# Performance work log

Measured on AMD Instinct MI355X. Metric: run time of the kernel, lower is better.

## Reference

```python
import jax, jax.numpy as jnp
import numpy as np

B, N, C = 4, 100000, 64
S = 256            # img_size
RADIUS_PX = 1.5    # radius in pixels
K = 8              # points_per_pixel
GAMMA = 1.0
R_NDC = RADIUS_PX / S * 2.0  # radius in NDC, as in forward()


def setup_inputs() -> dict:
    key = jax.random.key(0)
    k1, k2 = jax.random.split(key)
    pts = jax.random.normal(k1, (B, N, 3), dtype=jnp.float32)
    features = jax.random.normal(k2, (B, N, C), dtype=jnp.float32)
    return {"pts": pts, "features": features}


def _rasterize_one(pts_b):
    # pts_b: (N,3) sign-flipped NDC points. Emulates pytorch3d rasterize_points:
    # per pixel keep the K nearest-in-z points whose NDC distance to the pixel
    # center is <= R_NDC (points with z < 0 are culled).
    x, y, z = pts_b[:, 0], pts_b[:, 1], pts_b[:, 2]
    # pytorch3d NDC->pixel: ndc = 1 - 2*(p+0.5)/S  =>  p = (1-ndc)*S/2 - 0.5
    px = (1.0 - x) * (S / 2.0) - 0.5
    py = (1.0 - y) * (S / 2.0) - 0.5
    offs = jnp.arange(-1, 3)  # 4-wide window fully covers a 1.5px radius
    cj = jnp.floor(px).astype(jnp.int32)[:, None] + offs  # (N,4) candidate cols
    ci = jnp.floor(py).astype(jnp.int32)[:, None] + offs  # (N,4) candidate rows
    cx = 1.0 - 2.0 * (cj.astype(pts_b.dtype) + 0.5) / S   # pixel-center NDC x
    cy = 1.0 - 2.0 * (ci.astype(pts_b.dtype) + 0.5) / S   # pixel-center NDC y
    d2 = (cy - y[:, None])[:, :, None] ** 2 + (cx - x[:, None])[:, None, :] ** 2  # (N,4,4)
    pid = ci[:, :, None] * S + cj[:, None, :]                                      # (N,4,4)
    inb = (ci[:, :, None] >= 0) & (ci[:, :, None] < S) & (cj[:, None, :] >= 0) & (cj[:, None, :] < S)
    valid = inb & (d2 <= R_NDC * R_NDC) & (z[:, None, None] >= 0.0)
    pid = jnp.where(valid, pid, S * S).reshape(-1)
    zc = jnp.where(valid, z[:, None, None], jnp.inf).reshape(-1)
    d2f = d2.reshape(-1)
    pidx = jnp.broadcast_to(jnp.arange(N, dtype=jnp.int32)[:, None, None], (N, 4, 4)).reshape(-1)
    order = jnp.lexsort((zc, pid))  # sort by pixel id, then depth (front first)
    pid_s, d2_s, pi_s = pid[order], d2f[order], pidx[order]
    seg_start = jnp.searchsorted(pid_s, pid_s, side='left')
    rank = jnp.arange(pid_s.shape[0]) - seg_start  # per-pixel z-rank
    keep = (pid_s < S * S) & (rank < K)
    pid_w = jnp.where(keep, pid_s, S * S)          # OOB index -> dropped by mode='drop'
    rank_w = jnp.where(keep, rank, 0)
    idx_buf = jnp.full((S * S, K), -1, jnp.int32).at[pid_w, rank_w].set(pi_s, mode='drop')
    d_buf = jnp.zeros((S * S, K), pts_b.dtype).at[pid_w, rank_w].set(d2_s, mode='drop')
    return idx_buf.reshape(S, S, K), d_buf.reshape(S, S, K)


def _forward(pts, features):
    # forward() flips x and y signs in-place
    pts = pts * jnp.array([-1.0, -1.0, 1.0], dtype=pts.dtype)
    idx, d2 = jax.vmap(_rasterize_one)(pts)        # (B,S,S,K) each
    dist = d2 / (R_NDC * R_NDC)
    alphas = 1.0 - jnp.clip(dist, 0.001, 1.0) ** (0.5 * GAMMA)  # .pow(0.5).pow(gamma)
    alphas = jnp.where(idx >= 0, alphas, 0.0)      # alpha_composite skips idx < 0
    trans = jnp.cumprod(1.0 - alphas, axis=-1)     # transmittance, front-to-back
    trans = jnp.concatenate([jnp.ones_like(trans[..., :1]), trans[..., :-1]], axis=-1)
    w = alphas * trans                             # (B,S,S,K) compositing weights
    gath = jax.vmap(lambda f, i: f[jnp.clip(i, 0)])(features, idx)  # (B,S,S,K,C)
    return jnp.einsum('bhwk,bhwkc->bchw', w, gath)  # (B,C,S,S)


def reference(pts, features):
    return _forward(pts, features)
```

## Files before the change

kernel.cpp:

```cpp
#include <hip/hip_runtime.h>
#include <stdint.h>

#pragma clang fp contract(off)

#define S 256
#define NPTS 100000
#define BATCH 4
#define CCH 64
#define K 8

static constexpr float R2 = 0.01171875f * 0.01171875f;
static constexpr unsigned long long SENT = 0xFFFFFFFFFFFFFFFFULL;

__global__ void scatter_kernel(const float* __restrict__ pts,
                               unsigned long long* __restrict__ keys) {
    int gid = blockIdx.x * blockDim.x + threadIdx.x;
    if (gid >= BATCH * NPTS) return;
    int b = gid / NPTS;
    int n = gid - b * NPTS;

    const float* p = pts + (size_t)gid * 3;
    float x = -p[0];
    float y = -p[1];
    float z = p[2];
    if (!(z >= 0.0f)) return;

    float px = (1.0f - x) * 128.0f - 0.5f;
    float py = (1.0f - y) * 128.0f - 0.5f;
    int cj0 = (int)floorf(px);
    int ci0 = (int)floorf(py);
    if (ci0 < -2 || ci0 > S || cj0 < -2 || cj0 > S) return;

    unsigned long long zkey =
        ((unsigned long long)__float_as_uint(z) << 32) | (unsigned int)n;
    unsigned long long* kb = keys + (size_t)b * S * S * K;

    for (int a = 0; a < 4; ++a) {
        int ci = ci0 - 1 + a;
        if (ci < 0 || ci >= S) continue;
        float cy = 1.0f - 2.0f * ((float)ci + 0.5f) / 256.0f;
        float dy = cy - y;
        float dy2 = dy * dy;
        for (int d = 0; d < 4; ++d) {
            int cj = cj0 - 1 + d;
            if (cj < 0 || cj >= S) continue;
            float cx = 1.0f - 2.0f * ((float)cj + 0.5f) / 256.0f;
            float dx = cx - x;
            float dx2 = dx * dx;
            float d2 = dy2 + dx2;
            if (d2 <= R2) {
                unsigned long long key = zkey;
                unsigned long long* slot = kb + (size_t)(ci * S + cj) * K;
                for (int s = 0; s < K; ++s) {
                    if (key == SENT) break;
                    unsigned long long old = atomicMin(&slot[s], key);
                    key = old > key ? old : key;
                }
            }
        }
    }
}

__global__ __launch_bounds__(256) void blend_kernel(
        const float* __restrict__ pts,
        const float* __restrict__ feat,
        const unsigned long long* __restrict__ keys,
        float* __restrict__ out) {
    int seg = blockIdx.x;
    int h   = blockIdx.y;
    int b   = blockIdx.z;
    int tid = threadIdx.x;
    int w0  = seg * 64;

    __shared__ float s_alpha[64][K + 1];
    __shared__ float s_wgt[64][K + 1];
    __shared__ int   s_idx[64][K + 1];
    __shared__ int   s_cnt[64];

    const unsigned long long* kb =
        keys + ((size_t)b * S * S + (size_t)h * S + w0) * K;
    const float* pb = pts + (size_t)b * NPTS * 3;

    for (int e = tid; e < 64 * K; e += 256) {
        int p = e >> 3;
        int k = e & 7;
        unsigned long long key = kb[(size_t)p * K + k];
        float alpha = 0.0f;
        int idx = -1;
        if (key != SENT) {
            idx = (int)(unsigned int)(key & 0xFFFFFFFFULL);
            float x = -pb[(size_t)idx * 3 + 0];
            float y = -pb[(size_t)idx * 3 + 1];
            int w = w0 + p;
            float cy = 1.0f - 2.0f * ((float)h + 0.5f) / 256.0f;
            float cx = 1.0f - 2.0f * ((float)w + 0.5f) / 256.0f;
            float dy = cy - y;
            float dx = cx - x;
            float d2 = dy * dy + dx * dx;
            float dist = d2 / R2;
            dist = fminf(fmaxf(dist, 0.001f), 1.0f);
            alpha = 1.0f - sqrtf(dist);
        }
        s_alpha[p][k] = alpha;
        s_idx[p][k] = idx;
    }
    __syncthreads();

    if (tid < 64) {
        float t = 1.0f;
        int cnt = 0;
        for (int k = 0; k < K; ++k) {
            int raw = s_idx[tid][k];
            float a = s_alpha[tid][k];
            s_wgt[tid][k] = a * t;
            t *= (1.0f - a);
            if (raw >= 0) cnt = k + 1;
            s_idx[tid][k] = raw < 0 ? 0 : raw;
        }
        s_cnt[tid] = cnt;
    }
    __syncthreads();

    int wave = tid >> 6;
    int lane = tid & 63;
    int pbase = wave * 16;

    int kmax = 0;
#pragma unroll
    for (int i = 0; i < 16; ++i) {
        int c = s_cnt[pbase + i];
        kmax = c > kmax ? c : kmax;
    }

    float acc[16];
#pragma unroll
    for (int i = 0; i < 16; ++i) acc[i] = 0.0f;

    const float* fbl = feat + (size_t)b * NPTS * CCH + lane;
    for (int k = 0; k < kmax; ++k) {
        float v[16];
#pragma unroll
        for (int i = 0; i < 16; ++i) {
            int idx = s_idx[pbase + i][k];
            v[i] = fbl[(size_t)idx << 6];
        }
#pragma unroll
        for (int i = 0; i < 16; ++i) {
            acc[i] += s_wgt[pbase + i][k] * v[i];
        }
    }

    size_t obase = (((size_t)b * CCH + lane) * S + h) * S + (size_t)(w0 + pbase);
    float4* o4 = (float4*)(out + obase);
#pragma unroll
    for (int q = 0; q < 4; ++q) {
        o4[q] = make_float4(acc[4 * q + 0], acc[4 * q + 1],
                            acc[4 * q + 2], acc[4 * q + 3]);
    }
}

extern "C" void kernel_launch(void* const* d_in, const int* in_sizes, int n_in,
                              void* d_out, int out_size, void* d_ws, size_t ws_size,
                              hipStream_t stream) {
    const float* pts  = (const float*)d_in[0];
    const float* feat = (const float*)d_in[1];
    float* out = (float*)d_out;

    unsigned long long* keys = (unsigned long long*)d_ws;
    size_t key_bytes = (size_t)BATCH * S * S * K * sizeof(unsigned long long);
    hipMemsetAsync(keys, 0xFF, key_bytes, stream);

    int total = BATCH * NPTS;
    scatter_kernel<<<(total + 255) / 256, 256, 0, stream>>>(pts, keys);

    dim3 grid(S / 64, S, BATCH);
    blend_kernel<<<grid, 256, 0, stream>>>(pts, feat, keys, out);
}
```

Measured before the change: 277.7 us.

## Parallelize scatter over 16 window cells and early-exit on full pixel slots

The scatter kernel now launches one thread per point-cell pair (16 per point) instead of looping over the 4x4 window inside one thread, which spreads the serial atomicMin insertion chains across more threads. It also adds a plain read of the last slot and skips the atomic insertion when that slot already holds a smaller key. Each point's coordinates are now loaded by 16 threads, and the pre-check reads a value that other threads may be changing. It is safe because slots only decrease, so any skipped key would have been rejected anyway.

```diff
diff --git a/kernel.cpp b/kernel.cpp
--- a/kernel.cpp
+++ b/kernel.cpp
@@ -12,14 +12,17 @@
 static constexpr float R2 = 0.01171875f * 0.01171875f;
 static constexpr unsigned long long SENT = 0xFFFFFFFFFFFFFFFFULL;
 
-__global__ void scatter_kernel(const float* __restrict__ pts,
-                               unsigned long long* __restrict__ keys) {
+__global__ __launch_bounds__(256) void scatter_kernel(
+        const float* __restrict__ pts,
+        unsigned long long* __restrict__ keys) {
     int gid = blockIdx.x * blockDim.x + threadIdx.x;
-    if (gid >= BATCH * NPTS) return;
-    int b = gid / NPTS;
-    int n = gid - b * NPTS;
+    if (gid >= BATCH * NPTS * 16) return;
+    int cell = gid & 15;
+    int pid  = gid >> 4;
+    int b = pid / NPTS;
+    int n = pid - b * NPTS;
 
-    const float* p = pts + (size_t)gid * 3;
+    const float* p = pts + (size_t)pid * 3;
     float x = -p[0];
     float y = -p[1];
     float z = p[2];
@@ -29,35 +32,29 @@
     float py = (1.0f - y) * 128.0f - 0.5f;
     int cj0 = (int)floorf(px);
     int ci0 = (int)floorf(py);
-    if (ci0 < -2 || ci0 > S || cj0 < -2 || cj0 > S) return;
 
-    unsigned long long zkey =
+    int ci = ci0 - 1 + (cell >> 2);
+    int cj = cj0 - 1 + (cell & 3);
+    if (ci < 0 || ci >= S || cj < 0 || cj >= S) return;
+
+    float cy = 1.0f - 2.0f * ((float)ci + 0.5f) / 256.0f;
+    float cx = 1.0f - 2.0f * ((float)cj + 0.5f) / 256.0f;
+    float dy = cy - y;
+    float dx = cx - x;
+    float d2 = dy * dy + dx * dx;
+    if (!(d2 <= R2)) return;
+
+    unsigned long long key =
         ((unsigned long long)__float_as_uint(z) << 32) | (unsigned int)n;
-    unsigned long long* kb = keys + (size_t)b * S * S * K;
+    unsigned long long* slot =
+        keys + ((size_t)b * S * S + (size_t)(ci * S + cj)) * K;
 
-    for (int a = 0; a < 4; ++a) {
-        int ci = ci0 - 1 + a;
-        if (ci < 0 || ci >= S) continue;
-        float cy = 1.0f - 2.0f * ((float)ci + 0.5f) / 256.0f;
-        float dy = cy - y;
-        float dy2 = dy * dy;
-        for (int d = 0; d < 4; ++d) {
-            int cj = cj0 - 1 + d;
-            if (cj < 0 || cj >= S) continue;
-            float cx = 1.0f - 2.0f * ((float)cj + 0.5f) / 256.0f;
-            float dx = cx - x;
-            float dx2 = dx * dx;
-            float d2 = dy2 + dx2;
-            if (d2 <= R2) {
-                unsigned long long key = zkey;
-                unsigned long long* slot = kb + (size_t)(ci * S + cj) * K;
-                for (int s = 0; s < K; ++s) {
-                    if (key == SENT) break;
-                    unsigned long long old = atomicMin(&slot[s], key);
-                    key = old > key ? old : key;
-                }
-            }
-        }
+    if (slot[K - 1] < key) return;
+
+    for (int s = 0; s < K; ++s) {
+        if (key == SENT) break;
+        unsigned long long old = atomicMin(&slot[s], key);
+        key = old > key ? old : key;
     }
 }
 
@@ -170,7 +167,7 @@
     size_t key_bytes = (size_t)BATCH * S * S * K * sizeof(unsigned long long);
     hipMemsetAsync(keys, 0xFF, key_bytes, stream);
 
-    int total = BATCH * NPTS;
+    int total = BATCH * NPTS * 16;
     scatter_kernel<<<(total + 255) / 256, 256, 0, stream>>>(pts, keys);
 
     dim3 grid(S / 64, S, BATCH);
```

Measured after the change: 274.2 us. No clear change (-1.3%).

## Replace per-pixel atomic top-K scatter with tile binning and shared-memory top-K

Applied to the files above, without the earlier changes.

The fill kernel now bins each visible point into 16x16 pixel tiles, using one atomic counter per tile and a fixed-capacity entry list. A single tile kernel loads its tile's entries into shared memory, builds the per-pixel K-nearest-in-z list in registers, computes compositing weights and gathers features. This removes the large key-buffer memset, the per-pixel chains of 64-bit atomicMin, and the global key round trip between kernels. In exchange, each pixel thread scans the tile's whole list serially, and any point beyond a tile's capacity of 768 entries is silently dropped.

```diff
diff --git a/kernel.cpp b/kernel.cpp
--- a/kernel.cpp
+++ b/kernel.cpp
@@ -9,11 +9,18 @@
 #define CCH 64
 #define K 8
 
+#define TILE 16
+#define TPB 16
+#define NTILES (BATCH * TPB * TPB)
+#define CAP 768
+
 static constexpr float R2 = 0.01171875f * 0.01171875f;
 static constexpr unsigned long long SENT = 0xFFFFFFFFFFFFFFFFULL;
 
-__global__ void scatter_kernel(const float* __restrict__ pts,
-                               unsigned long long* __restrict__ keys) {
+__global__ __launch_bounds__(256) void fill_kernel(
+        const float* __restrict__ pts,
+        int* __restrict__ counts,
+        float4* __restrict__ entries) {
     int gid = blockIdx.x * blockDim.x + threadIdx.x;
     if (gid >= BATCH * NPTS) return;
     int b = gid / NPTS;
@@ -29,133 +36,144 @@
     float py = (1.0f - y) * 128.0f - 0.5f;
     int cj0 = (int)floorf(px);
     int ci0 = (int)floorf(py);
-    if (ci0 < -2 || ci0 > S || cj0 < -2 || cj0 > S) return;
+    if (ci0 + 2 < 0 || ci0 - 1 > S - 1 || cj0 + 2 < 0 || cj0 - 1 > S - 1) return;
 
-    unsigned long long zkey =
-        ((unsigned long long)__float_as_uint(z) << 32) | (unsigned int)n;
-    unsigned long long* kb = keys + (size_t)b * S * S * K;
+    int ti_lo = (ci0 - 1 < 0 ? 0 : ci0 - 1) >> 4;
+    int ti_hi = (ci0 + 2 > S - 1 ? S - 1 : ci0 + 2) >> 4;
+    int tj_lo = (cj0 - 1 < 0 ? 0 : cj0 - 1) >> 4;
+    int tj_hi = (cj0 + 2 > S - 1 ? S - 1 : cj0 + 2) >> 4;
 
-    for (int a = 0; a < 4; ++a) {
-        int ci = ci0 - 1 + a;
-        if (ci < 0 || ci >= S) continue;
-        float cy = 1.0f - 2.0f * ((float)ci + 0.5f) / 256.0f;
-        float dy = cy - y;
-        float dy2 = dy * dy;
-        for (int d = 0; d < 4; ++d) {
-            int cj = cj0 - 1 + d;
-            if (cj < 0 || cj >= S) continue;
-            float cx = 1.0f - 2.0f * ((float)cj + 0.5f) / 256.0f;
-            float dx = cx - x;
-            float dx2 = dx * dx;
-            float d2 = dy2 + dx2;
-            if (d2 <= R2) {
-                unsigned long long key = zkey;
-                unsigned long long* slot = kb + (size_t)(ci * S + cj) * K;
-                for (int s = 0; s < K; ++s) {
-                    if (key == SENT) break;
-                    unsigned long long old = atomicMin(&slot[s], key);
-                    key = old > key ? old : key;
-                }
-            }
+    float4 v = make_float4(x, y, z, __int_as_float(n));
+    for (int ti = ti_lo; ti <= ti_hi; ++ti) {
+        for (int tj = tj_lo; tj <= tj_hi; ++tj) {
+            int t = (b * TPB + ti) * TPB + tj;
+            int pos = atomicAdd(&counts[t], 1);
+            if (pos < CAP) entries[(size_t)t * CAP + pos] = v;
         }
     }
 }
 
-__global__ __launch_bounds__(256) void blend_kernel(
-        const float* __restrict__ pts,
+__global__ __launch_bounds__(512) void tile_kernel(
         const float* __restrict__ feat,
-        const unsigned long long* __restrict__ keys,
+        const int* __restrict__ counts,
+        const float4* __restrict__ entries,
         float* __restrict__ out) {
-    int seg = blockIdx.x;
-    int h   = blockIdx.y;
-    int b   = blockIdx.z;
+    int tj = blockIdx.x;
+    int ti = blockIdx.y;
+    int b  = blockIdx.z;
     int tid = threadIdx.x;
-    int w0  = seg * 64;
 
-    __shared__ float s_alpha[64][K + 1];
-    __shared__ float s_wgt[64][K + 1];
-    __shared__ int   s_idx[64][K + 1];
-    __shared__ int   s_cnt[64];
+    __shared__ float4 s_ent[CAP];
+    __shared__ uint2  s_slots[TILE * TILE][K];
+    __shared__ int    s_cnt[TILE * TILE];
 
-    const unsigned long long* kb =
-        keys + ((size_t)b * S * S + (size_t)h * S + w0) * K;
-    const float* pb = pts + (size_t)b * NPTS * 3;
+    int t = (b * TPB + ti) * TPB + tj;
+    int cnt = counts[t];
+    if (cnt > CAP) cnt = CAP;
+    const float4* elist = entries + (size_t)t * CAP;
 
-    for (int e = tid; e < 64 * K; e += 256) {
-        int p = e >> 3;
-        int k = e & 7;
-        unsigned long long key = kb[(size_t)p * K + k];
-        float alpha = 0.0f;
-        int idx = -1;
-        if (key != SENT) {
-            idx = (int)(unsigned int)(key & 0xFFFFFFFFULL);
-            float x = -pb[(size_t)idx * 3 + 0];
-            float y = -pb[(size_t)idx * 3 + 1];
-            int w = w0 + p;
-            float cy = 1.0f - 2.0f * ((float)h + 0.5f) / 256.0f;
-            float cx = 1.0f - 2.0f * ((float)w + 0.5f) / 256.0f;
-            float dy = cy - y;
-            float dx = cx - x;
-            float d2 = dy * dy + dx * dx;
-            float dist = d2 / R2;
-            dist = fminf(fmaxf(dist, 0.001f), 1.0f);
-            alpha = 1.0f - sqrtf(dist);
-        }
-        s_alpha[p][k] = alpha;
-        s_idx[p][k] = idx;
-    }
+    for (int i = tid; i < cnt; i += 512) s_ent[i] = elist[i];
     __syncthreads();
 
-    if (tid < 64) {
-        float t = 1.0f;
-        int cnt = 0;
+    if (tid < TILE * TILE) {
+        int pi = tid;
+        int h = ti * TILE + (pi >> 4);
+        int w = tj * TILE + (pi & 15);
+        float cy = 1.0f - 2.0f * ((float)h + 0.5f) / 256.0f;
+        float cx = 1.0f - 2.0f * ((float)w + 0.5f) / 256.0f;
+
+        unsigned long long topk[K];
+        float topd2[K];
+#pragma unroll
+        for (int k = 0; k < K; ++k) { topk[k] = SENT; topd2[k] = 0.0f; }
+
+        for (int e = 0; e < cnt; ++e) {
+            float4 v = s_ent[e];
+            float dy = cy - v.y;
+            float dx = cx - v.x;
+            float d2 = dy * dy + dx * dx;
+            if (d2 <= R2) {
+                unsigned long long key =
+                    ((unsigned long long)__float_as_uint(v.z) << 32) |
+                    (unsigned int)__float_as_int(v.w);
+                if (key < topk[K - 1]) {
+#pragma unroll
+                    for (int k = K - 1; k >= 0; --k) {
+                        unsigned long long cur = topk[k];
+                        float curd = topd2[k];
+                        bool prev_ge = (k > 0) && (topk[k - 1] > key);
+                        bool cur_ge = (cur > key);
+                        unsigned long long pk = (k > 0) ? topk[k - 1] : 0ULL;
+                        float pd = (k > 0) ? topd2[k - 1] : 0.0f;
+                        topk[k]  = prev_ge ? pk : (cur_ge ? key : cur);
+                        topd2[k] = prev_ge ? pd : (cur_ge ? d2 : curd);
+                    }
+                }
+            }
+        }
+
+        float trans = 1.0f;
+        int cnt_p = 0;
+#pragma unroll
         for (int k = 0; k < K; ++k) {
-            int raw = s_idx[tid][k];
-            float a = s_alpha[tid][k];
-            s_wgt[tid][k] = a * t;
-            t *= (1.0f - a);
-            if (raw >= 0) cnt = k + 1;
-            s_idx[tid][k] = raw < 0 ? 0 : raw;
+            unsigned long long key = topk[k];
+            float wgt = 0.0f;
+            unsigned idx = 0;
+            if (key != SENT) {
+                idx = (unsigned)(key & 0xFFFFFFFFULL);
+                float dist = topd2[k] / R2;
+                dist = fminf(fmaxf(dist, 0.001f), 1.0f);
+                float alpha = 1.0f - sqrtf(dist);
+                wgt = alpha * trans;
+                trans *= (1.0f - alpha);
+                cnt_p = k + 1;
+            }
+            s_slots[pi][k] = make_uint2(idx, __float_as_uint(wgt));
         }
-        s_cnt[tid] = cnt;
+        s_cnt[pi] = cnt_p;
     }
     __syncthreads();
 
     int wave = tid >> 6;
     int lane = tid & 63;
-    int pbase = wave * 16;
+    const float* fbl = feat + (size_t)b * NPTS * CCH + lane;
 
-    int kmax = 0;
-#pragma unroll
-    for (int i = 0; i < 16; ++i) {
-        int c = s_cnt[pbase + i];
-        kmax = c > kmax ? c : kmax;
-    }
+    for (int rr = 0; rr < 2; ++rr) {
+        int r = wave * 2 + rr;
+        int pbase = r * TILE;
 
-    float acc[16];
-#pragma unroll
-    for (int i = 0; i < 16; ++i) acc[i] = 0.0f;
-
-    const float* fbl = feat + (size_t)b * NPTS * CCH + lane;
-    for (int k = 0; k < kmax; ++k) {
-        float v[16];
+        int kmax = 0;
 #pragma unroll
         for (int i = 0; i < 16; ++i) {
-            int idx = s_idx[pbase + i][k];
-            v[i] = fbl[(size_t)idx << 6];
+            int c = s_cnt[pbase + i];
+            kmax = c > kmax ? c : kmax;
         }
+
+        float acc[16];
 #pragma unroll
-        for (int i = 0; i < 16; ++i) {
-            acc[i] += s_wgt[pbase + i][k] * v[i];
+        for (int i = 0; i < 16; ++i) acc[i] = 0.0f;
+
+        for (int k = 0; k < kmax; ++k) {
+            float vv[16];
+            float ww[16];
+#pragma unroll
+            for (int i = 0; i < 16; ++i) {
+                uint2 u = s_slots[pbase + i][k];
+                ww[i] = __uint_as_float(u.y);
+                vv[i] = fbl[(size_t)u.x << 6];
+            }
+#pragma unroll
+            for (int i = 0; i < 16; ++i) acc[i] += ww[i] * vv[i];
         }
-    }
 
-    size_t obase = (((size_t)b * CCH + lane) * S + h) * S + (size_t)(w0 + pbase);
-    float4* o4 = (float4*)(out + obase);
+        int h = ti * TILE + r;
+        int w0 = tj * TILE;
+        size_t obase = (((size_t)b * CCH + lane) * S + h) * S + w0;
+        float4* o4 = (float4*)(out + obase);
 #pragma unroll
-    for (int q = 0; q < 4; ++q) {
-        o4[q] = make_float4(acc[4 * q + 0], acc[4 * q + 1],
-                            acc[4 * q + 2], acc[4 * q + 3]);
+        for (int q = 0; q < 4; ++q)
+            o4[q] = make_float4(acc[4 * q + 0], acc[4 * q + 1],
+                                acc[4 * q + 2], acc[4 * q + 3]);
     }
 }
 
@@ -166,13 +184,14 @@
     const float* feat = (const float*)d_in[1];
     float* out = (float*)d_out;
 
-    unsigned long long* keys = (unsigned long long*)d_ws;
-    size_t key_bytes = (size_t)BATCH * S * S * K * sizeof(unsigned long long);
-    hipMemsetAsync(keys, 0xFF, key_bytes, stream);
+    int* counts = (int*)d_ws;
+    float4* entries = (float4*)((char*)d_ws + 4096);
+
+    hipMemsetAsync(counts, 0, NTILES * sizeof(int), stream);
 
     int total = BATCH * NPTS;
-    scatter_kernel<<<(total + 255) / 256, 256, 0, stream>>>(pts, keys);
+    fill_kernel<<<(total + 255) / 256, 256, 0, stream>>>(pts, counts, entries);
 
-    dim3 grid(S / 64, S, BATCH);
-    blend_kernel<<<grid, 256, 0, stream>>>(pts, feat, keys, out);
+    dim3 grid(TPB, TPB, BATCH);
+    tile_kernel<<<grid, 512, 0, stream>>>(feat, counts, entries, out);
 }
```

New measurement: 275.8 us. About the same (-0.7%).
